# Performance work log

Measured on AMD Instinct MI355X. Metric: run time of the kernel, lower is better.

## Reference

```python
import jax, jax.numpy as jnp
import numpy as np

B, T, C = 2, 2048, 1024
H = 16
D = C // H  # head_dim = 64


def setup_inputs() -> dict:
    key = jax.random.key(0)
    k1, k2, k3 = jax.random.split(key, 3)
    x = jax.random.normal(k1, (B, T, C), dtype=jnp.float32)
    # causal mask: True means 'mask out' (masked_fill semantics)
    attn_mask = jnp.triu(jnp.ones((T, T), dtype=bool), k=1)[None, None]
    W_attn = jax.random.normal(k2, (C, 3 * C), dtype=jnp.float32) * (1.0 / np.sqrt(C))
    b_attn = jnp.zeros((3 * C,), dtype=jnp.float32)
    W_proj = jax.random.normal(k3, (C, C), dtype=jnp.float32) * (1.0 / np.sqrt(C))
    b_proj = jnp.zeros((C,), dtype=jnp.float32)
    return {"x": x, "attn_mask": attn_mask, "W_attn": W_attn, "b_attn": b_attn,
            "W_proj": W_proj, "b_proj": b_proj}


def reference(x, attn_mask, W_attn, b_attn, W_proj, b_proj):
    Bb, Tt, Cc = x.shape
    qkv = x @ W_attn + b_attn                      # [B,T,3C]
    q, k, v = jnp.split(qkv, 3, axis=-1)
    def to_heads(t):
        return t.reshape(Bb, Tt, H, D).transpose(0, 2, 1, 3)  # [B,H,T,D]
    q, k, v = to_heads(q), to_heads(k), to_heads(v)
    scale = 1.0 / np.sqrt(D).astype(np.float32)
    attn = jnp.einsum('bhqd,bhkd->bhqk', q, k) * scale  # [B,H,T,T]
    attn = jnp.where(attn_mask, -jnp.inf, attn)
    attn = jax.nn.softmax(attn, axis=-1)
    y = jnp.einsum('bhqk,bhkd->bhqd', attn, v)          # [B,H,T,D]
    y = y.transpose(0, 2, 1, 3).reshape(Bb, Tt, Cc)
    return y @ W_proj + b_proj
```

## Files before the change

kernel.cpp:

```cpp
#include <hip/hip_runtime.h>
#include <math.h>


#define TSEQ 2048
#define NHD  16
#define DH   64
#define CDIM 1024

typedef __attribute__((ext_vector_type(8))) short bf16x8;
typedef __attribute__((ext_vector_type(4))) float f32x4;

#define MFMA(a, b, c) __builtin_amdgcn_mfma_f32_16x16x32_bf16((a), (b), (c), 0, 0, 0)

__device__ __forceinline__ ushort f2bf(float f) {
    unsigned u = __builtin_bit_cast(unsigned, f);
    u += 0x7FFFu + ((u >> 16) & 1u);
    return (ushort)(u >> 16);
}
__device__ __forceinline__ float bf2f(ushort h) {
    unsigned u = ((unsigned)h) << 16;
    return __builtin_bit_cast(float, u);
}

__global__ __launch_bounds__(256) void cast_k(const float* __restrict__ in,
                                              ushort* __restrict__ out, int n4) {
    int i = blockIdx.x * 256 + threadIdx.x;
    const int stride = gridDim.x * 256;
    for (; i < n4; i += stride) {
        float4 f = ((const float4*)in)[i];
        ushort4 o;
        o.x = f2bf(f.x); o.y = f2bf(f.y); o.z = f2bf(f.z); o.w = f2bf(f.w);
        ((ushort4*)out)[i] = o;
    }
}

__global__ __launch_bounds__(256) void transpose_k(const float* __restrict__ in,
                                                   ushort* __restrict__ out,
                                                   int R, int C) {
    __shared__ float t[32][33];
    const int tx = threadIdx.x, ty = threadIdx.y;
    const int c0 = blockIdx.x * 32, r0 = blockIdx.y * 32;
#pragma unroll
    for (int i = 0; i < 4; ++i)
        t[ty + i * 8][tx] = in[(size_t)(r0 + ty + i * 8) * C + c0 + tx];
    __syncthreads();
#pragma unroll
    for (int i = 0; i < 4; ++i)
        out[(size_t)(c0 + ty + i * 8) * R + r0 + tx] = f2bf(t[tx][ty + i * 8]);
}

__global__ __launch_bounds__(256) void qkv_k(const ushort* __restrict__ X,
                                             const ushort* __restrict__ Wt,
                                             const float* __restrict__ bias,
                                             ushort* __restrict__ qb,
                                             ushort* __restrict__ kb,
                                             ushort* __restrict__ vtb) {
    const int fid = blockIdx.x;
    const int nf = (fid & 7) * 96 + (fid >> 3);
    const int mt = nf / 24, nt = nf % 24;
    const int m0 = mt * 128, n0 = nt * 128;
    const int tid = threadIdx.x, lane = tid & 63, w = tid >> 6;
    const int l15 = lane & 15, g = lane >> 4;
    const int wm = w >> 1, wn = w & 1;

    const ushort* Ar[4]; const ushort* Br[4];
#pragma unroll
    for (int s = 0; s < 4; ++s) {
        Ar[s] = X  + (size_t)(m0 + wm * 64 + s * 16 + l15) * 1024 + g * 8;
        Br[s] = Wt + (size_t)(n0 + wn * 64 + s * 16 + l15) * 1024 + g * 8;
    }
    f32x4 acc[4][4] = {};
    bf16x8 a[4], b[4], a2[4], b2[4];
#pragma unroll
    for (int s = 0; s < 4; ++s) { a[s] = *(const bf16x8*)(Ar[s]); b[s] = *(const bf16x8*)(Br[s]); }

    for (int kk = 0; kk < 1024; kk += 32) {
        if (kk + 32 < 1024) {
#pragma unroll
            for (int s = 0; s < 4; ++s) {
                a2[s] = *(const bf16x8*)(Ar[s] + kk + 32);
                b2[s] = *(const bf16x8*)(Br[s] + kk + 32);
            }
        }
#pragma unroll
        for (int i = 0; i < 4; ++i)
#pragma unroll
            for (int j = 0; j < 4; ++j)
                acc[i][j] = MFMA(a[i], b[j], acc[i][j]);
#pragma unroll
        for (int s = 0; s < 4; ++s) { a[s] = a2[s]; b[s] = b2[s]; }
    }
#pragma unroll
    for (int j = 0; j < 4; ++j) {
        const int n = n0 + wn * 64 + j * 16 + l15;
        const float bv = bias[n];
        const int which = n >> 10;
        const int c = n & 1023, h = c >> 6, d = c & 63;
#pragma unroll
        for (int i = 0; i < 4; ++i)
#pragma unroll
            for (int r = 0; r < 4; ++r) {
                const int m = m0 + wm * 64 + i * 16 + g * 4 + r;
                const int bb = m >> 11, t = m & 2047;
                const float val = acc[i][j][r] + bv;
                const int bh = bb * NHD + h;
                if (which == 0)
                    qb[((size_t)bh * TSEQ + t) * 64 + d] = f2bf(val * 0.125f);
                else if (which == 1)
                    kb[((size_t)bh * TSEQ + t) * 64 + d] = f2bf(val);
                else
                    vtb[((size_t)bh * 64 + d) * TSEQ + t] = f2bf(val);
            }
    }
}

__global__ __launch_bounds__(64, 4) void attn_k(const ushort* __restrict__ Q,
                                                const ushort* __restrict__ K,
                                                const ushort* __restrict__ VT,
                                                ushort* __restrict__ Yh,
                                                ushort* __restrict__ Yl) {
    __shared__ ushort P[16][72];
    const int fid = blockIdx.x;
    const int nf = (fid & 7) * 512 + (fid >> 3);
    const int bh = nf >> 7, q16 = nf & 127;
    const int lane = threadIdx.x & 63;
    const int l15 = lane & 15, g = lane >> 4;
    const int q0 = q16 * 16;

    const ushort* Qb = Q  + (size_t)bh * TSEQ * 64;
    const ushort* Kb = K  + (size_t)bh * TSEQ * 64;
    const ushort* Vb = VT + (size_t)bh * 64 * TSEQ;

    bf16x8 qf0 = *(const bf16x8*)(Qb + (size_t)(q0 + l15) * 64 + g * 8);
    bf16x8 qf1 = *(const bf16x8*)(Qb + (size_t)(q0 + l15) * 64 + 32 + g * 8);

    f32x4 o[4] = {};
    float m_run = -INFINITY, l_run = 0.f;
    const int nT = (q0 + 15) / 64 + 1;

    bf16x8 ak[4][2], ak2[4][2], av[4][2];
#pragma unroll
    for (int s = 0; s < 4; ++s) {
        const ushort* kr = Kb + (size_t)(s * 16 + l15) * 64 + g * 8;
        ak[s][0] = *(const bf16x8*)(kr);
        ak[s][1] = *(const bf16x8*)(kr + 32);
    }

    for (int t = 0; t < nT; ++t) {
        const int kv0 = t * 64;
#pragma unroll
        for (int s = 0; s < 4; ++s) {
            const ushort* vr = Vb + (size_t)(s * 16 + l15) * TSEQ + kv0 + g * 8;
            av[s][0] = *(const bf16x8*)(vr);
            av[s][1] = *(const bf16x8*)(vr + 32);
        }
        if (t + 1 < nT) {
#pragma unroll
            for (int s = 0; s < 4; ++s) {
                const ushort* kr = Kb + (size_t)(kv0 + 64 + s * 16 + l15) * 64 + g * 8;
                ak2[s][0] = *(const bf16x8*)(kr);
                ak2[s][1] = *(const bf16x8*)(kr + 32);
            }
        }
        f32x4 s4[4] = {};
#pragma unroll
        for (int s = 0; s < 4; ++s) {
            s4[s] = MFMA(ak[s][0], qf0, s4[s]);
            s4[s] = MFMA(ak[s][1], qf1, s4[s]);
        }
        if (kv0 + 63 > q0) {
#pragma unroll
            for (int s = 0; s < 4; ++s)
#pragma unroll
                for (int r = 0; r < 4; ++r) {
                    const int kg = kv0 + s * 16 + g * 4 + r;
                    if (kg > q0 + l15) s4[s][r] = -INFINITY;
                }
        }
        float mx = -INFINITY;
#pragma unroll
        for (int s = 0; s < 4; ++s)
#pragma unroll
            for (int r = 0; r < 4; ++r) mx = fmaxf(mx, s4[s][r]);
        mx = fmaxf(mx, __shfl_xor(mx, 16));
        mx = fmaxf(mx, __shfl_xor(mx, 32));
        const float mnew = fmaxf(m_run, mx);
        const float alpha = __expf(m_run - mnew);
        float lsum = 0.f;
#pragma unroll
        for (int s = 0; s < 4; ++s) {
            float p0 = __expf(s4[s][0] - mnew);
            float p1 = __expf(s4[s][1] - mnew);
            float p2 = __expf(s4[s][2] - mnew);
            float p3 = __expf(s4[s][3] - mnew);
            lsum += (p0 + p1) + (p2 + p3);
            ushort4 pw;
            pw.x = f2bf(p0); pw.y = f2bf(p1); pw.z = f2bf(p2); pw.w = f2bf(p3);
            *(ushort4*)&P[l15][s * 16 + g * 4] = pw;
        }
        lsum += __shfl_xor(lsum, 16);
        lsum += __shfl_xor(lsum, 32);
        l_run = l_run * alpha + lsum;
        m_run = mnew;
#pragma unroll
        for (int s = 0; s < 4; ++s)
#pragma unroll
            for (int r = 0; r < 4; ++r) o[s][r] *= alpha;
        bf16x8 pb0 = *(const bf16x8*)&P[l15][g * 8];
        bf16x8 pb1 = *(const bf16x8*)&P[l15][32 + g * 8];
#pragma unroll
        for (int s = 0; s < 4; ++s) {
            o[s] = MFMA(av[s][0], pb0, o[s]);
            o[s] = MFMA(av[s][1], pb1, o[s]);
        }
#pragma unroll
        for (int s = 0; s < 4; ++s) { ak[s][0] = ak2[s][0]; ak[s][1] = ak2[s][1]; }
    }
    const float inv = 1.f / l_run;
    const int t = q0 + l15;
    const size_t base = ((size_t)(bh >> 4) * TSEQ + t) * CDIM + (bh & 15) * 64;
#pragma unroll
    for (int s = 0; s < 4; ++s) {
        ushort4 hv, lv;
        float v;
        v = o[s][0] * inv; hv.x = f2bf(v); lv.x = f2bf(v - bf2f(hv.x));
        v = o[s][1] * inv; hv.y = f2bf(v); lv.y = f2bf(v - bf2f(hv.y));
        v = o[s][2] * inv; hv.z = f2bf(v); lv.z = f2bf(v - bf2f(hv.z));
        v = o[s][3] * inv; hv.w = f2bf(v); lv.w = f2bf(v - bf2f(hv.w));
        *(ushort4*)&Yh[base + s * 16 + g * 4] = hv;
        *(ushort4*)&Yl[base + s * 16 + g * 4] = lv;
    }
}

__global__ __launch_bounds__(256) void proj_k(const ushort* __restrict__ Yh,
                                              const ushort* __restrict__ Yl,
                                              const ushort* __restrict__ Wt,
                                              const float* __restrict__ bias,
                                              float* __restrict__ out) {
    const int fid = blockIdx.x;
    const int nf = (fid & 7) * 32 + (fid >> 3);
    const int mt = nf >> 3, nt = nf & 7;
    const int m0 = mt * 128, n0 = nt * 128;
    const int tid = threadIdx.x, lane = tid & 63, w = tid >> 6;
    const int l15 = lane & 15, g = lane >> 4;
    const int wm = w >> 1, wn = w & 1;

    const ushort* Ah[4]; const ushort* Al[4]; const ushort* Br[4];
#pragma unroll
    for (int s = 0; s < 4; ++s) {
        const size_t arow = (size_t)(m0 + wm * 64 + s * 16 + l15) * 1024 + g * 8;
        Ah[s] = Yh + arow;
        Al[s] = Yl + arow;
        Br[s] = Wt + (size_t)(n0 + wn * 64 + s * 16 + l15) * 1024 + g * 8;
    }
    f32x4 acc[4][4] = {};
#pragma unroll 2
    for (int kk = 0; kk < 1024; kk += 32) {
        bf16x8 ah[4], al[4], b[4];
#pragma unroll
        for (int s = 0; s < 4; ++s) {
            ah[s] = *(const bf16x8*)(Ah[s] + kk);
            al[s] = *(const bf16x8*)(Al[s] + kk);
            b[s]  = *(const bf16x8*)(Br[s] + kk);
        }
#pragma unroll
        for (int i = 0; i < 4; ++i)
#pragma unroll
            for (int j = 0; j < 4; ++j) {
                acc[i][j] = MFMA(ah[i], b[j], acc[i][j]);
                acc[i][j] = MFMA(al[i], b[j], acc[i][j]);
            }
    }
#pragma unroll
    for (int j = 0; j < 4; ++j) {
        const int n = n0 + wn * 64 + j * 16 + l15;
        const float bv = bias[n];
#pragma unroll
        for (int i = 0; i < 4; ++i)
#pragma unroll
            for (int r = 0; r < 4; ++r) {
                const int m = m0 + wm * 64 + i * 16 + g * 4 + r;
                out[(size_t)m * 1024 + n] = acc[i][j][r] + bv;
            }
    }
}

extern "C" void kernel_launch(void* const* d_in, const int* in_sizes, int n_in,
                              void* d_out, int out_size, void* d_ws, size_t ws_size,
                              hipStream_t stream) {
    (void)in_sizes; (void)n_in; (void)out_size; (void)ws_size;
    const float* x      = (const float*)d_in[0];
    const float* W_attn = (const float*)d_in[2];
    const float* b_attn = (const float*)d_in[3];
    const float* W_proj = (const float*)d_in[4];
    const float* b_proj = (const float*)d_in[5];
    float* out = (float*)d_out;

    ushort* xb  = (ushort*)d_ws;
    ushort* wta = xb  + 4194304;
    ushort* wtp = wta + 3145728;
    ushort* qb  = wtp + 1048576;
    ushort* kb  = qb  + 4194304;
    ushort* vtb = kb  + 4194304;
    ushort* yh  = vtb + 4194304;
    ushort* yl  = yh  + 4194304;

    cast_k<<<1024, 256, 0, stream>>>(x, xb, 4194304 / 4);
    transpose_k<<<dim3(96, 32), dim3(32, 8), 0, stream>>>(W_attn, wta, 1024, 3072);
    transpose_k<<<dim3(32, 32), dim3(32, 8), 0, stream>>>(W_proj, wtp, 1024, 1024);
    qkv_k<<<768, 256, 0, stream>>>(xb, wta, b_attn, qb, kb, vtb);
    attn_k<<<4096, 64, 0, stream>>>(qb, kb, vtb, yh, yl);
    proj_k<<<256, 256, 0, stream>>>(yh, yl, wtp, b_proj, out);
}
```

Measured before the change: 406.0 us.

## Split attention KV range across four waves and split-K the output projection

The attention kernel now runs four waves per 16-query block. Each wave handles every fourth 64-key tile, and the partial max, sum and output are merged through shared memory with a log-sum-exp combine. The projection kernel uses 64x64 tiles with four-way split-K across waves, reduced serially in shared memory, and writes coalesced float4 rows. Both changes aim to shorten the serial per-block critical path and raise wave parallelism. The cost is extra LDS traffic, a barrier, and idle waves for early query blocks that have few KV tiles.

After: 635.5 us. 56.5% more time.

```diff
diff --git a/kernel.cpp b/kernel.cpp
--- a/kernel.cpp
+++ b/kernel.cpp
@@ -114,16 +114,20 @@
     }
 }
 
-__global__ __launch_bounds__(64, 4) void attn_k(const ushort* __restrict__ Q,
-                                                const ushort* __restrict__ K,
-                                                const ushort* __restrict__ VT,
-                                                ushort* __restrict__ Yh,
-                                                ushort* __restrict__ Yl) {
-    __shared__ ushort P[16][72];
+__global__ __launch_bounds__(256, 6) void attn_k(const ushort* __restrict__ Q,
+                                                 const ushort* __restrict__ K,
+                                                 const ushort* __restrict__ VT,
+                                                 ushort* __restrict__ Yh,
+                                                 ushort* __restrict__ Yl) {
+    __shared__ ushort P[4][16][72];
+    __shared__ float Om[4][16][66];
+    __shared__ float Mw[4][16];
+    __shared__ float Lw[4][16];
+
     const int fid = blockIdx.x;
     const int nf = (fid & 7) * 512 + (fid >> 3);
     const int bh = nf >> 7, q16 = nf & 127;
-    const int lane = threadIdx.x & 63;
+    const int tid = threadIdx.x, w = tid >> 6, lane = tid & 63;
     const int l15 = lane & 15, g = lane >> 4;
     const int q0 = q16 * 16;
 
@@ -136,17 +140,19 @@
 
     f32x4 o[4] = {};
     float m_run = -INFINITY, l_run = 0.f;
-    const int nT = (q0 + 15) / 64 + 1;
+    const int nT = q0 / 64 + 1;
 
     bf16x8 ak[4][2], ak2[4][2], av[4][2];
-#pragma unroll
-    for (int s = 0; s < 4; ++s) {
-        const ushort* kr = Kb + (size_t)(s * 16 + l15) * 64 + g * 8;
-        ak[s][0] = *(const bf16x8*)(kr);
-        ak[s][1] = *(const bf16x8*)(kr + 32);
-    }
-
-    for (int t = 0; t < nT; ++t) {
+    if (w < nT) {
+#pragma unroll
+        for (int s = 0; s < 4; ++s) {
+            const ushort* kr = Kb + (size_t)(w * 64 + s * 16 + l15) * 64 + g * 8;
+            ak[s][0] = *(const bf16x8*)(kr);
+            ak[s][1] = *(const bf16x8*)(kr + 32);
+        }
+    }
+
+    for (int t = w; t < nT; t += 4) {
         const int kv0 = t * 64;
 #pragma unroll
         for (int s = 0; s < 4; ++s) {
@@ -154,10 +160,10 @@
             av[s][0] = *(const bf16x8*)(vr);
             av[s][1] = *(const bf16x8*)(vr + 32);
         }
-        if (t + 1 < nT) {
+        if (t + 4 < nT) {
 #pragma unroll
             for (int s = 0; s < 4; ++s) {
-                const ushort* kr = Kb + (size_t)(kv0 + 64 + s * 16 + l15) * 64 + g * 8;
+                const ushort* kr = Kb + (size_t)(kv0 + 256 + s * 16 + l15) * 64 + g * 8;
                 ak2[s][0] = *(const bf16x8*)(kr);
                 ak2[s][1] = *(const bf16x8*)(kr + 32);
             }
@@ -196,7 +202,7 @@
             lsum += (p0 + p1) + (p2 + p3);
             ushort4 pw;
             pw.x = f2bf(p0); pw.y = f2bf(p1); pw.z = f2bf(p2); pw.w = f2bf(p3);
-            *(ushort4*)&P[l15][s * 16 + g * 4] = pw;
+            *(ushort4*)&P[w][l15][s * 16 + g * 4] = pw;
         }
         lsum += __shfl_xor(lsum, 16);
         lsum += __shfl_xor(lsum, 32);
@@ -206,8 +212,8 @@
         for (int s = 0; s < 4; ++s)
 #pragma unroll
             for (int r = 0; r < 4; ++r) o[s][r] *= alpha;
-        bf16x8 pb0 = *(const bf16x8*)&P[l15][g * 8];
-        bf16x8 pb1 = *(const bf16x8*)&P[l15][32 + g * 8];
+        bf16x8 pb0 = *(const bf16x8*)&P[w][l15][g * 8];
+        bf16x8 pb1 = *(const bf16x8*)&P[w][l15][32 + g * 8];
 #pragma unroll
         for (int s = 0; s < 4; ++s) {
             o[s] = MFMA(av[s][0], pb0, o[s]);
@@ -216,46 +222,67 @@
 #pragma unroll
         for (int s = 0; s < 4; ++s) { ak[s][0] = ak2[s][0]; ak[s][1] = ak2[s][1]; }
     }
-    const float inv = 1.f / l_run;
-    const int t = q0 + l15;
-    const size_t base = ((size_t)(bh >> 4) * TSEQ + t) * CDIM + (bh & 15) * 64;
+
+    if (g == 0) { Mw[w][l15] = m_run; Lw[w][l15] = l_run; }
 #pragma unroll
     for (int s = 0; s < 4; ++s) {
-        ushort4 hv, lv;
-        float v;
-        v = o[s][0] * inv; hv.x = f2bf(v); lv.x = f2bf(v - bf2f(hv.x));
-        v = o[s][1] * inv; hv.y = f2bf(v); lv.y = f2bf(v - bf2f(hv.y));
-        v = o[s][2] * inv; hv.z = f2bf(v); lv.z = f2bf(v - bf2f(hv.z));
-        v = o[s][3] * inv; hv.w = f2bf(v); lv.w = f2bf(v - bf2f(hv.w));
-        *(ushort4*)&Yh[base + s * 16 + g * 4] = hv;
-        *(ushort4*)&Yl[base + s * 16 + g * 4] = lv;
-    }
-}
-
-__global__ __launch_bounds__(256) void proj_k(const ushort* __restrict__ Yh,
-                                              const ushort* __restrict__ Yl,
-                                              const ushort* __restrict__ Wt,
-                                              const float* __restrict__ bias,
-                                              float* __restrict__ out) {
+        *(float2*)&Om[w][l15][s * 16 + g * 4]     = make_float2(o[s][0], o[s][1]);
+        *(float2*)&Om[w][l15][s * 16 + g * 4 + 2] = make_float2(o[s][2], o[s][3]);
+    }
+    __syncthreads();
+
+    const float m0v = Mw[0][l15], m1v = Mw[1][l15], m2v = Mw[2][l15], m3v = Mw[3][l15];
+    const float m_tot = fmaxf(fmaxf(m0v, m1v), fmaxf(m2v, m3v));
+    float l_tot = 0.f;
+    f32x4 od = {};
+#pragma unroll
+    for (int j = 0; j < 4; ++j) {
+        const float sc = __expf(Mw[j][l15] - m_tot);
+        l_tot += Lw[j][l15] * sc;
+        const float2 p0 = *(const float2*)&Om[j][l15][w * 16 + g * 4];
+        const float2 p1 = *(const float2*)&Om[j][l15][w * 16 + g * 4 + 2];
+        od[0] += p0.x * sc; od[1] += p0.y * sc;
+        od[2] += p1.x * sc; od[3] += p1.y * sc;
+    }
+    const float inv = 1.f / l_tot;
+    const int trow = q0 + l15;
+    const size_t base = ((size_t)(bh >> 4) * TSEQ + trow) * CDIM + (bh & 15) * 64
+                        + w * 16 + g * 4;
+    ushort4 hv, lv;
+    float v;
+    v = od[0] * inv; hv.x = f2bf(v); lv.x = f2bf(v - bf2f(hv.x));
+    v = od[1] * inv; hv.y = f2bf(v); lv.y = f2bf(v - bf2f(hv.y));
+    v = od[2] * inv; hv.z = f2bf(v); lv.z = f2bf(v - bf2f(hv.z));
+    v = od[3] * inv; hv.w = f2bf(v); lv.w = f2bf(v - bf2f(hv.w));
+    *(ushort4*)&Yh[base] = hv;
+    *(ushort4*)&Yl[base] = lv;
+}
+
+__global__ __launch_bounds__(256, 3) void proj_k(const ushort* __restrict__ Yh,
+                                                 const ushort* __restrict__ Yl,
+                                                 const ushort* __restrict__ Wt,
+                                                 const float* __restrict__ bias,
+                                                 float* __restrict__ out) {
+    __shared__ float S[64][68];
     const int fid = blockIdx.x;
-    const int nf = (fid & 7) * 32 + (fid >> 3);
-    const int mt = nf >> 3, nt = nf & 7;
-    const int m0 = mt * 128, n0 = nt * 128;
-    const int tid = threadIdx.x, lane = tid & 63, w = tid >> 6;
+    const int nf = (fid & 7) * 128 + (fid >> 3);
+    const int mt = nf >> 4, nt = nf & 15;
+    const int m0 = mt * 64, n0 = nt * 64;
+    const int tid = threadIdx.x, w = tid >> 6, lane = tid & 63;
     const int l15 = lane & 15, g = lane >> 4;
-    const int wm = w >> 1, wn = w & 1;
+    const int k0 = w * 256;
 
     const ushort* Ah[4]; const ushort* Al[4]; const ushort* Br[4];
 #pragma unroll
     for (int s = 0; s < 4; ++s) {
-        const size_t arow = (size_t)(m0 + wm * 64 + s * 16 + l15) * 1024 + g * 8;
+        const size_t arow = (size_t)(m0 + s * 16 + l15) * 1024 + k0 + g * 8;
         Ah[s] = Yh + arow;
         Al[s] = Yl + arow;
-        Br[s] = Wt + (size_t)(n0 + wn * 64 + s * 16 + l15) * 1024 + g * 8;
+        Br[s] = Wt + (size_t)(n0 + s * 16 + l15) * 1024 + k0 + g * 8;
     }
     f32x4 acc[4][4] = {};
 #pragma unroll 2
-    for (int kk = 0; kk < 1024; kk += 32) {
+    for (int kk = 0; kk < 256; kk += 32) {
         bf16x8 ah[4], al[4], b[4];
 #pragma unroll
         for (int s = 0; s < 4; ++s) {
@@ -271,17 +298,31 @@
                 acc[i][j] = MFMA(al[i], b[j], acc[i][j]);
             }
     }
-#pragma unroll
-    for (int j = 0; j < 4; ++j) {
-        const int n = n0 + wn * 64 + j * 16 + l15;
-        const float bv = bias[n];
-#pragma unroll
-        for (int i = 0; i < 4; ++i)
-#pragma unroll
-            for (int r = 0; r < 4; ++r) {
-                const int m = m0 + wm * 64 + i * 16 + g * 4 + r;
-                out[(size_t)m * 1024 + n] = acc[i][j][r] + bv;
-            }
+    for (int ww = 0; ww < 4; ++ww) {
+        if (ww == w) {
+#pragma unroll
+            for (int i = 0; i < 4; ++i)
+#pragma unroll
+                for (int j = 0; j < 4; ++j) {
+                    f32x4* dst = (f32x4*)&S[j * 16 + l15][i * 16 + g * 4];
+                    if (ww == 0) *dst = acc[i][j];
+                    else         *dst = *dst + acc[i][j];
+                }
+        }
+        __syncthreads();
+    }
+    const int m = tid >> 2;
+    const int nq = (tid & 3) * 16;
+    float* orow = out + (size_t)(m0 + m) * 1024 + n0 + nq;
+#pragma unroll
+    for (int u = 0; u < 16; u += 4) {
+        const float4 bv = *(const float4*)&bias[n0 + nq + u];
+        float4 vo;
+        vo.x = S[nq + u + 0][m] + bv.x;
+        vo.y = S[nq + u + 1][m] + bv.y;
+        vo.z = S[nq + u + 2][m] + bv.z;
+        vo.w = S[nq + u + 3][m] + bv.w;
+        *(float4*)&orow[u] = vo;
     }
 }
 
@@ -309,6 +350,6 @@
     transpose_k<<<dim3(96, 32), dim3(32, 8), 0, stream>>>(W_attn, wta, 1024, 3072);
     transpose_k<<<dim3(32, 32), dim3(32, 8), 0, stream>>>(W_proj, wtp, 1024, 1024);
     qkv_k<<<768, 256, 0, stream>>>(xb, wta, b_attn, qb, kb, vtb);
-    attn_k<<<4096, 64, 0, stream>>>(qb, kb, vtb, yh, yl);
-    proj_k<<<256, 256, 0, stream>>>(yh, yl, wtp, b_proj, out);
-}
+    attn_k<<<4096, 256, 0, stream>>>(qb, kb, vtb, yh, yl);
+    proj_k<<<1024, 256, 0, stream>>>(yh, yl, wtp, b_proj, out);
+}
```
